# Kernel optimization log

Hardware: AMD Instinct MI355X
Metric: run time of the kernel (lower is better)

Reference implementation:

```python
import math
import jax, jax.numpy as jnp
import numpy as np

DIM = 128
NUM_PROJ = 256
B, H, SEQ = 2, 16, 4096


def _make_orthogonal_S(key):
    # Mirrors QJLWithOrthogonal.__init__: raw Gaussian, QR-orthogonalize each
    # dim-row chunk, scale by sqrt(dim).
    raw = jax.random.normal(key, (NUM_PROJ, DIM), dtype=jnp.float32)
    blocks = []
    for start in range(0, NUM_PROJ, DIM):
        block = raw[start:min(start + DIM, NUM_PROJ)]
        if block.shape[0] <= block.shape[1]:
            q, _ = jnp.linalg.qr(block.T)  # reduced QR of [dim, rows]
            blocks.append(q.T * np.float32(math.sqrt(DIM)))
        else:
            blocks.append(block)
    return jnp.concatenate(blocks, axis=0)[:NUM_PROJ]


def setup_inputs() -> dict:
    key = jax.random.key(0)
    kq, kk, ks = jax.random.split(key, 3)
    query = jax.random.normal(kq, (B, H, SEQ, DIM), dtype=jnp.float32)
    key_t = jax.random.normal(kk, (B, H, SEQ, DIM), dtype=jnp.float32)
    S = _make_orthogonal_S(ks)
    return {"query": query, "key": key_t, "S": S}


def reference(query, key, S):
    # quantize(key): sign of JL projection -> {-1, +1}, shape [B,H,S,m]
    z = jnp.sign(jnp.einsum('bhsd,md->bhsm', key, S))
    # estimate_inner_product(query, z): asymmetric estimator
    qp = jnp.einsum('bhsd,md->bhsm', query, S)
    scale = np.float32(math.sqrt(math.pi / 2) / NUM_PROJ)
    return scale * jnp.sum(qp * z, axis=-1)  # [B,H,S]
```

## Files before the change

kernel.cpp:

```cpp
#include <hip/hip_runtime.h>
#include <hip/hip_bf16.h>


#define DIM        128
#define NPROJ      256
#define TILE_T     32
#define NWG        4096
#define LDS_STRIDE 136
#define TAU        6.0e-3f
#define SCALE      0.0048957583489668f

typedef __attribute__((ext_vector_type(8))) short short8;
typedef __attribute__((ext_vector_type(4))) float f32x4;

static __device__ __forceinline__ unsigned short bf16_rne(float x){
    unsigned int u = __builtin_bit_cast(unsigned int, x);
    u += 0x7FFFu + ((u >> 16) & 1u);
    return (unsigned short)(u >> 16);
}

static __device__ __attribute__((noinline))
float ref_sign(const float* __restrict__ Kg, const float* __restrict__ S,
               int tok, int m){
    const float* kr = Kg + (size_t)tok * DIM;
    const float* sr = S  + (size_t)m   * DIM;
    float acc = 0.f;
#pragma unroll 8
    for (int d = 0; d < DIM; ++d)
        acc = __builtin_fmaf(kr[d], sr[d], acc);
    return (acc > 0.f) ? 1.f : ((acc < 0.f) ? -1.f : 0.f);
}

__global__ void prep_s_kernel(const float* __restrict__ S,
                              unsigned short* __restrict__ shi,
                              unsigned short* __restrict__ slo){
    int t    = blockIdx.x * 256 + threadIdx.x;
    int lane = t & 63;
    int ms   = (t >> 6) & 3;
    int ks   = (t >> 8) & 3;
    int g    = (t >> 10) & 3;
    int m    = g*64 + ms*16 + (lane & 15);
    int d    = ks*32 + (lane >> 4)*8;
    const float4* p = (const float4*)(S + (size_t)m*DIM + d);
    float4 x0 = p[0], x1 = p[1];
    float xs[8] = {x0.x,x0.y,x0.z,x0.w, x1.x,x1.y,x1.z,x1.w};
    size_t base = ((size_t)t) * 8;
    unsigned long long h0=0,h1=0,l0=0,l1=0;
#pragma unroll
    for (int e = 0; e < 4; ++e){
        unsigned short hb = bf16_rne(xs[e]);
        float hf = __builtin_bit_cast(float, (unsigned int)hb << 16);
        h0 |= (unsigned long long)hb                    << (16*e);
        l0 |= (unsigned long long)bf16_rne(xs[e] - hf)  << (16*e);
    }
#pragma unroll
    for (int e = 0; e < 4; ++e){
        unsigned short hb = bf16_rne(xs[4+e]);
        float hf = __builtin_bit_cast(float, (unsigned int)hb << 16);
        h1 |= (unsigned long long)hb                      << (16*e);
        l1 |= (unsigned long long)bf16_rne(xs[4+e] - hf)  << (16*e);
    }
    *(unsigned long long*)(shi + base)     = h0;
    *(unsigned long long*)(shi + base + 4) = h1;
    *(unsigned long long*)(slo + base)     = l0;
    *(unsigned long long*)(slo + base + 4) = l1;
}

template<bool USE_TAB>
static __device__ __forceinline__
void load_afrags(const unsigned short* __restrict__ shi_tab,
                 const unsigned short* __restrict__ slo_tab,
                 const float* __restrict__ S,
                 int wave, int ks, int l16, int quad, int lane,
                 short8 ah[4], short8 al[4], bool need_lo){
    if (USE_TAB){
#pragma unroll
        for (int ms = 0; ms < 4; ++ms){
            size_t off = ((size_t)((wave*4 + ks)*4 + ms)*64 + lane)*8;
            ah[ms] = *(const short8*)(shi_tab + off);
            if (need_lo) al[ms] = *(const short8*)(slo_tab + off);
        }
    } else {
#pragma unroll
        for (int ms = 0; ms < 4; ++ms){
            const float4* p = (const float4*)(S + (size_t)(wave*64 + ms*16 + l16)*DIM
                                              + ks*32 + quad*8);
            float4 x0 = p[0], x1 = p[1];
            float xs[8] = {x0.x,x0.y,x0.z,x0.w, x1.x,x1.y,x1.z,x1.w};
            short8 h, l;
#pragma unroll
            for (int e = 0; e < 8; ++e){
                unsigned short hb = bf16_rne(xs[e]);
                float hf = __builtin_bit_cast(float, (unsigned int)hb << 16);
                h[e] = (short)hb;
                l[e] = (short)bf16_rne(xs[e] - hf);
            }
            ah[ms] = h;
            if (need_lo) al[ms] = l;
        }
    }
}

template<bool USE_TAB>
__global__ __launch_bounds__(256, 4)
void qjl_kernel(const float* __restrict__ Qg, const float* __restrict__ Kg,
                const float* __restrict__ S,
                const unsigned short* __restrict__ shi_tab,
                const unsigned short* __restrict__ slo_tab,
                float* __restrict__ out)
{
    __shared__ unsigned short khi[TILE_T * LDS_STRIDE];
    __shared__ unsigned short klo[TILE_T * LDS_STRIDE];
    __shared__ unsigned short qhi[TILE_T * LDS_STRIDE];
    __shared__ float red[4][TILE_T];

    const int tid  = threadIdx.x;
    const int wave = tid >> 6;
    const int lane = tid & 63;
    const int l16  = lane & 15;
    const int quad = lane >> 4;
    const int tok0 = blockIdx.x * TILE_T;

    {
        const float4* ksrc = (const float4*)(Kg + (size_t)tok0 * DIM);
        const float4* qsrc = (const float4*)(Qg + (size_t)tok0 * DIM);
        float4 kv[4], qv[4];
#pragma unroll
        for (int j = 0; j < 4; ++j){ kv[j] = ksrc[tid + j*256]; qv[j] = qsrc[tid + j*256]; }
#pragma unroll
        for (int j = 0; j < 4; ++j){
            int i   = tid + j*256;
            int row = i >> 5;
            int c   = i & 31;
            float kx[4] = {kv[j].x, kv[j].y, kv[j].z, kv[j].w};
            float qx[4] = {qv[j].x, qv[j].y, qv[j].z, qv[j].w};
            unsigned long long hp = 0, lp = 0, qp = 0;
#pragma unroll
            for (int e = 0; e < 4; ++e){
                unsigned short hb = bf16_rne(kx[e]);
                float hf = __builtin_bit_cast(float, (unsigned int)hb << 16);
                hp |= (unsigned long long)hb                   << (16*e);
                lp |= (unsigned long long)bf16_rne(kx[e] - hf) << (16*e);
                qp |= (unsigned long long)bf16_rne(qx[e])      << (16*e);
            }
            int base = row * LDS_STRIDE + c*4;
            *(unsigned long long*)(khi + base) = hp;
            *(unsigned long long*)(klo + base) = lp;
            *(unsigned long long*)(qhi + base) = qp;
        }
    }
    __syncthreads();

    unsigned int negw = 0, zerow = 0;
    {
        f32x4 accC[4][2];
#pragma unroll
        for (int ms = 0; ms < 4; ++ms)
#pragma unroll
            for (int ts = 0; ts < 2; ++ts)
                accC[ms][ts] = (f32x4){0.f,0.f,0.f,0.f};

#pragma unroll
        for (int ks = 0; ks < 4; ++ks){
            short8 ah[4], al[4];
            load_afrags<USE_TAB>(shi_tab, slo_tab, S, wave, ks, l16, quad, lane,
                                 ah, al, true);
#pragma unroll
            for (int ts = 0; ts < 2; ++ts){
                const int off = (ts*16 + l16) * LDS_STRIDE + ks*32 + quad*8;
                short8 bk = *(const short8*)(khi + off);
                short8 bl = *(const short8*)(klo + off);
#pragma unroll
                for (int ms = 0; ms < 4; ++ms){
                    accC[ms][ts] = __builtin_amdgcn_mfma_f32_16x16x32_bf16(ah[ms], bk, accC[ms][ts], 0,0,0);
                    accC[ms][ts] = __builtin_amdgcn_mfma_f32_16x16x32_bf16(al[ms], bk, accC[ms][ts], 0,0,0);
                    accC[ms][ts] = __builtin_amdgcn_mfma_f32_16x16x32_bf16(ah[ms], bl, accC[ms][ts], 0,0,0);
                }
            }
        }
#pragma unroll
        for (int ts = 0; ts < 2; ++ts){
#pragma unroll
            for (int ms = 0; ms < 4; ++ms){
#pragma unroll
                for (int r = 0; r < 4; ++r){
                    float c = accC[ms][ts][r];
                    float s = (c >= 0.f) ? 1.f : -1.f;
                    if (__builtin_fabsf(c) < TAU)
                        s = ref_sign(Kg, S, tok0 + ts*16 + l16,
                                     wave*64 + ms*16 + quad*4 + r);
                    int bit = (ts*4 + ms)*4 + r;
                    if (s < 0.f)  negw  |= (1u << bit);
                    if (s == 0.f) zerow |= (1u << bit);
                }
            }
        }
    }

    float part0 = 0.f, part1 = 0.f;
    {
        f32x4 accQ[4][2];
#pragma unroll
        for (int ms = 0; ms < 4; ++ms)
#pragma unroll
            for (int ts = 0; ts < 2; ++ts)
                accQ[ms][ts] = (f32x4){0.f,0.f,0.f,0.f};

#pragma unroll
        for (int ks = 0; ks < 4; ++ks){
            short8 ah[4], al_unused[4];
            load_afrags<USE_TAB>(shi_tab, slo_tab, S, wave, ks, l16, quad, lane,
                                 ah, al_unused, false);
#pragma unroll
            for (int ts = 0; ts < 2; ++ts){
                const int off = (ts*16 + l16) * LDS_STRIDE + ks*32 + quad*8;
                short8 bq = *(const short8*)(qhi + off);
#pragma unroll
                for (int ms = 0; ms < 4; ++ms)
                    accQ[ms][ts] = __builtin_amdgcn_mfma_f32_16x16x32_bf16(ah[ms], bq, accQ[ms][ts], 0,0,0);
            }
        }
#pragma unroll
        for (int ts = 0; ts < 2; ++ts){
#pragma unroll
            for (int ms = 0; ms < 4; ++ms){
#pragma unroll
                for (int r = 0; r < 4; ++r){
                    float qp = accQ[ms][ts][r];
                    int bit = (ts*4 + ms)*4 + r;
                    float sv = (zerow >> bit) & 1u ? 0.f
                             : ((negw >> bit) & 1u ? -qp : qp);
                    if (ts) part1 += sv; else part0 += sv;
                }
            }
        }
    }

    part0 += __shfl_xor(part0, 16, 64);
    part0 += __shfl_xor(part0, 32, 64);
    part1 += __shfl_xor(part1, 16, 64);
    part1 += __shfl_xor(part1, 32, 64);
    if (quad == 0){
        red[wave][l16]      = part0;
        red[wave][16 + l16] = part1;
    }
    __syncthreads();
    if (tid < TILE_T)
        out[tok0 + tid] = SCALE * (red[0][tid] + red[1][tid] + red[2][tid] + red[3][tid]);
}

extern "C" void kernel_launch(void* const* d_in, const int* in_sizes, int n_in,
                              void* d_out, int out_size, void* d_ws, size_t ws_size,
                              hipStream_t stream){
    const float* Qg = (const float*)d_in[0];
    const float* Kg = (const float*)d_in[1];
    const float* S  = (const float*)d_in[2];
    float* out = (float*)d_out;

    const size_t tab_elems = (size_t)NPROJ * DIM;
    const size_t need = 2 * tab_elems * sizeof(unsigned short);

    if (d_ws && ws_size >= need){
        unsigned short* shi = (unsigned short*)d_ws;
        unsigned short* slo = shi + tab_elems;
        prep_s_kernel<<<16, 256, 0, stream>>>(S, shi, slo);
        qjl_kernel<true><<<NWG, 256, 0, stream>>>(Qg, Kg, S, shi, slo, out);
    } else {
        qjl_kernel<false><<<NWG, 256, 0, stream>>>(Qg, Kg, S, nullptr, nullptr, out);
    }
}
```

Baseline: 206.6 us.

## Fuse key and query projection MFMA loops sharing S fragment loads

Merges the key-sign and query-projection passes into one k-loop, so each S A-fragment (hi/lo) is loaded once and feeds both accumulator sets. The sign/zero bitmask is dropped and the sign multiplies the query projection directly in the epilogue. The rare exact-sign fallback now uses float4 vector loads. Holding both accumulator sets live raises register pressure, which can lower occupancy under the 256x4 launch bound.

Measured after the change: 184.4 us. -10.8%, faster.

```diff
diff --git a/kernel.cpp b/kernel.cpp
--- a/kernel.cpp
+++ b/kernel.cpp
@@ -22,12 +22,18 @@
 static __device__ __attribute__((noinline))
 float ref_sign(const float* __restrict__ Kg, const float* __restrict__ S,
                int tok, int m){
-    const float* kr = Kg + (size_t)tok * DIM;
-    const float* sr = S  + (size_t)m   * DIM;
+    const float4* kr = (const float4*)(Kg + (size_t)tok * DIM);
+    const float4* sr = (const float4*)(S  + (size_t)m   * DIM);
     float acc = 0.f;
-#pragma unroll 8
-    for (int d = 0; d < DIM; ++d)
-        acc = __builtin_fmaf(kr[d], sr[d], acc);
+#pragma unroll 4
+    for (int d = 0; d < DIM/4; ++d){
+        float4 k4 = kr[d];
+        float4 s4 = sr[d];
+        acc = __builtin_fmaf(k4.x, s4.x, acc);
+        acc = __builtin_fmaf(k4.y, s4.y, acc);
+        acc = __builtin_fmaf(k4.z, s4.z, acc);
+        acc = __builtin_fmaf(k4.w, s4.w, acc);
+    }
     return (acc > 0.f) ? 1.f : ((acc < 0.f) ? -1.f : 0.f);
 }
 
@@ -72,13 +78,13 @@
                  const unsigned short* __restrict__ slo_tab,
                  const float* __restrict__ S,
                  int wave, int ks, int l16, int quad, int lane,
-                 short8 ah[4], short8 al[4], bool need_lo){
+                 short8 ah[4], short8 al[4]){
     if (USE_TAB){
 #pragma unroll
         for (int ms = 0; ms < 4; ++ms){
             size_t off = ((size_t)((wave*4 + ks)*4 + ms)*64 + lane)*8;
             ah[ms] = *(const short8*)(shi_tab + off);
-            if (need_lo) al[ms] = *(const short8*)(slo_tab + off);
+            al[ms] = *(const short8*)(slo_tab + off);
         }
     } else {
 #pragma unroll
@@ -96,7 +102,7 @@
                 l[e] = (short)bf16_rne(xs[e] - hf);
             }
             ah[ms] = h;
-            if (need_lo) al[ms] = l;
+            al[ms] = l;
         }
     }
 }
@@ -151,87 +157,51 @@
     }
     __syncthreads();
 
-    unsigned int negw = 0, zerow = 0;
-    {
-        f32x4 accC[4][2];
-#pragma unroll
-        for (int ms = 0; ms < 4; ++ms)
-#pragma unroll
-            for (int ts = 0; ts < 2; ++ts)
-                accC[ms][ts] = (f32x4){0.f,0.f,0.f,0.f};
-
-#pragma unroll
-        for (int ks = 0; ks < 4; ++ks){
-            short8 ah[4], al[4];
-            load_afrags<USE_TAB>(shi_tab, slo_tab, S, wave, ks, l16, quad, lane,
-                                 ah, al, true);
-#pragma unroll
-            for (int ts = 0; ts < 2; ++ts){
-                const int off = (ts*16 + l16) * LDS_STRIDE + ks*32 + quad*8;
-                short8 bk = *(const short8*)(khi + off);
-                short8 bl = *(const short8*)(klo + off);
-#pragma unroll
-                for (int ms = 0; ms < 4; ++ms){
-                    accC[ms][ts] = __builtin_amdgcn_mfma_f32_16x16x32_bf16(ah[ms], bk, accC[ms][ts], 0,0,0);
-                    accC[ms][ts] = __builtin_amdgcn_mfma_f32_16x16x32_bf16(al[ms], bk, accC[ms][ts], 0,0,0);
-                    accC[ms][ts] = __builtin_amdgcn_mfma_f32_16x16x32_bf16(ah[ms], bl, accC[ms][ts], 0,0,0);
-                }
-            }
-        }
+    f32x4 accC[4][2];
+    f32x4 accQ[4][2];
+#pragma unroll
+    for (int ms = 0; ms < 4; ++ms)
 #pragma unroll
         for (int ts = 0; ts < 2; ++ts){
+            accC[ms][ts] = (f32x4){0.f,0.f,0.f,0.f};
+            accQ[ms][ts] = (f32x4){0.f,0.f,0.f,0.f};
+        }
+
+#pragma unroll
+    for (int ks = 0; ks < 4; ++ks){
+        short8 ah[4], al[4];
+        load_afrags<USE_TAB>(shi_tab, slo_tab, S, wave, ks, l16, quad, lane,
+                             ah, al);
+#pragma unroll
+        for (int ts = 0; ts < 2; ++ts){
+            const int off = (ts*16 + l16) * LDS_STRIDE + ks*32 + quad*8;
+            short8 bk = *(const short8*)(khi + off);
+            short8 bl = *(const short8*)(klo + off);
+            short8 bq = *(const short8*)(qhi + off);
 #pragma unroll
             for (int ms = 0; ms < 4; ++ms){
-#pragma unroll
-                for (int r = 0; r < 4; ++r){
-                    float c = accC[ms][ts][r];
-                    float s = (c >= 0.f) ? 1.f : -1.f;
-                    if (__builtin_fabsf(c) < TAU)
-                        s = ref_sign(Kg, S, tok0 + ts*16 + l16,
-                                     wave*64 + ms*16 + quad*4 + r);
-                    int bit = (ts*4 + ms)*4 + r;
-                    if (s < 0.f)  negw  |= (1u << bit);
-                    if (s == 0.f) zerow |= (1u << bit);
-                }
+                accC[ms][ts] = __builtin_amdgcn_mfma_f32_16x16x32_bf16(ah[ms], bk, accC[ms][ts], 0,0,0);
+                accC[ms][ts] = __builtin_amdgcn_mfma_f32_16x16x32_bf16(al[ms], bk, accC[ms][ts], 0,0,0);
+                accC[ms][ts] = __builtin_amdgcn_mfma_f32_16x16x32_bf16(ah[ms], bl, accC[ms][ts], 0,0,0);
+                accQ[ms][ts] = __builtin_amdgcn_mfma_f32_16x16x32_bf16(ah[ms], bq, accQ[ms][ts], 0,0,0);
             }
         }
     }
 
     float part0 = 0.f, part1 = 0.f;
-    {
-        f32x4 accQ[4][2];
-#pragma unroll
-        for (int ms = 0; ms < 4; ++ms)
-#pragma unroll
-            for (int ts = 0; ts < 2; ++ts)
-                accQ[ms][ts] = (f32x4){0.f,0.f,0.f,0.f};
-
-#pragma unroll
-        for (int ks = 0; ks < 4; ++ks){
-            short8 ah[4], al_unused[4];
-            load_afrags<USE_TAB>(shi_tab, slo_tab, S, wave, ks, l16, quad, lane,
-                                 ah, al_unused, false);
-#pragma unroll
-            for (int ts = 0; ts < 2; ++ts){
-                const int off = (ts*16 + l16) * LDS_STRIDE + ks*32 + quad*8;
-                short8 bq = *(const short8*)(qhi + off);
-#pragma unroll
-                for (int ms = 0; ms < 4; ++ms)
-                    accQ[ms][ts] = __builtin_amdgcn_mfma_f32_16x16x32_bf16(ah[ms], bq, accQ[ms][ts], 0,0,0);
-            }
-        }
-#pragma unroll
-        for (int ts = 0; ts < 2; ++ts){
-#pragma unroll
-            for (int ms = 0; ms < 4; ++ms){
-#pragma unroll
-                for (int r = 0; r < 4; ++r){
-                    float qp = accQ[ms][ts][r];
-                    int bit = (ts*4 + ms)*4 + r;
-                    float sv = (zerow >> bit) & 1u ? 0.f
-                             : ((negw >> bit) & 1u ? -qp : qp);
-                    if (ts) part1 += sv; else part0 += sv;
-                }
+#pragma unroll
+    for (int ts = 0; ts < 2; ++ts){
+#pragma unroll
+        for (int ms = 0; ms < 4; ++ms){
+#pragma unroll
+            for (int r = 0; r < 4; ++r){
+                float c = accC[ms][ts][r];
+                float s = (c >= 0.f) ? 1.f : -1.f;
+                if (__builtin_fabsf(c) < TAU)
+                    s = ref_sign(Kg, S, tok0 + ts*16 + l16,
+                                 wave*64 + ms*16 + quad*4 + r);
+                float sv = s * accQ[ms][ts][r];
+                if (ts) part1 += sv; else part0 += sv;
             }
         }
     }
```
